# Kernel optimization log

Hardware: AMD Instinct MI355X
Metric: run time of the kernel (lower is better)

Reference implementation:

```python
import jax, jax.numpy as jnp
import numpy as np

B, TGT, SRC, H = 32, 512, 2048, 512


def setup_inputs() -> dict:
    key = jax.random.key(0)
    k1, k2, k3, k4, k5 = jax.random.split(key, 5)
    s = 1.0 / np.sqrt(H)
    return {
        "decoder_output": jax.random.normal(k1, (B, TGT, H), jnp.float32),
        "encoder_outputs": jax.random.normal(k2, (B, SRC, H), jnp.float32),
        # lengths in [SRC//2, SRC] so every row has at least one valid position
        "encoder_inputs_length": jax.random.randint(k3, (B,), SRC // 2, SRC + 1, jnp.int64),
        "W_in": jax.random.normal(k4, (H, H), jnp.float32) * s,   # linear_in weight (general)
        "W_out": jax.random.normal(k5, (H, 2 * H), jnp.float32) * s,  # linear_out weight, no bias
    }


def reference(decoder_output, encoder_outputs, encoder_inputs_length, W_in, W_out):
    # score (general): (q @ W_in^T) @ enc^T -> [B, tgt, src]
    q = jnp.einsum('bth,oh->bto', decoder_output, W_in)
    align = jnp.einsum('bth,bsh->bts', q, encoder_outputs)
    # mask positions j >= length with -inf, then softmax over src dim
    mask = jnp.arange(SRC)[None, None, :] < encoder_inputs_length[:, None, None]  # [B,1,src]
    align = jnp.where(mask, align, -jnp.inf)
    align_vectors = jax.nn.softmax(align, axis=2)  # [B, tgt, src]
    # context: [B, tgt, H]
    context = jnp.einsum('bts,bsh->bth', align_vectors, encoder_outputs)
    concat = jnp.concatenate([context, decoder_output], axis=2)  # [B, tgt, 2H]
    attn_h = jnp.tanh(jnp.einsum('btk,ok->bto', concat, W_out))  # [B, tgt, H]
    # transpose to [tgt, B, ...] as the torch module does
    return attn_h.transpose(1, 0, 2), align_vectors.transpose(1, 0, 2)
```

## Files before the change

kernel.cpp:

```cpp
#include <hip/hip_runtime.h>

#define Bc   32
#define TGTc 512
#define SRCc 2048
#define Hc   512

typedef unsigned short u16;
typedef unsigned int   u32;
typedef __attribute__((ext_vector_type(8))) short s16x8;
typedef __attribute__((ext_vector_type(4))) float f32x4;
typedef __attribute__((ext_vector_type(4))) unsigned short u16x4;

__device__ __forceinline__ u16 f2bf(float x) {
    u32 u = __float_as_uint(x);
    u32 r = (u + 0x7FFFu + ((u >> 16) & 1u)) >> 16;
    return (u16)r;
}
__device__ __forceinline__ float bf2f(u16 h) {
    return __uint_as_float(((u32)h) << 16);
}


__global__ void prep_len_k(const u32* __restrict__ raw, int* __restrict__ out) {
    int i = threadIdx.x;
    if (i >= Bc) return;
    bool is64 = (raw[1] == 0u);
    out[i] = (int)(is64 ? raw[2 * i] : raw[i]);
}

__global__ __launch_bounds__(256) void split_k(const float* __restrict__ in,
                                               u16* __restrict__ hi, u16* __restrict__ lo,
                                               int n4) {
    int stride = gridDim.x * 256;
    for (int i = blockIdx.x * 256 + threadIdx.x; i < n4; i += stride) {
        f32x4 x = ((const f32x4*)in)[i];
        u16x4 h, l;
#pragma unroll
        for (int j = 0; j < 4; j++) {
            u16 hb = f2bf(x[j]);
            h[j] = hb;
            l[j] = f2bf(x[j] - bf2f(hb));
        }
        ((u16x4*)hi)[i] = h;
        ((u16x4*)lo)[i] = l;
    }
}

__global__ __launch_bounds__(256) void split_wout_k(const float* __restrict__ in,
                                                    u16* __restrict__ ah, u16* __restrict__ al,
                                                    u16* __restrict__ bh, u16* __restrict__ bl) {
    int i = blockIdx.x * 256 + threadIdx.x;
    if (i >= 512 * 256) return;
    int o = i >> 8, kc = i & 255;
    f32x4 x = ((const f32x4*)in)[i];
    u16x4 h, l;
#pragma unroll
    for (int j = 0; j < 4; j++) {
        u16 hb = f2bf(x[j]);
        h[j] = hb;
        l[j] = f2bf(x[j] - bf2f(hb));
    }
    int half = kc >> 7;
    int idx = o * 128 + (kc & 127);
    ((u16x4*)(half ? bh : ah))[idx] = h;
    ((u16x4*)(half ? bl : al))[idx] = l;
}

__global__ __launch_bounds__(256) void prep_enc_k(const float* __restrict__ enc,
                                                  u16* __restrict__ ehi, u16* __restrict__ elo,
                                                  u16* __restrict__ ethi) {
    __shared__ float tile[32][33];
    const int b = blockIdx.z;
    const int s0 = blockIdx.x << 5, h0 = blockIdx.y << 5;
    const int x = threadIdx.x & 31, y = threadIdx.x >> 5;
    const long base = ((long)b * SRCc + s0) * Hc + h0;
#pragma unroll
    for (int j = 0; j < 4; j++) {
        int s = (y << 2) + j;
        float v = enc[base + (long)s * Hc + x];
        tile[s][x] = v;
        u16 h = f2bf(v);
        long o = base + (long)s * Hc + x;
        ehi[o] = h;
        elo[o] = f2bf(v - bf2f(h));
    }
    __syncthreads();
    const long tbase = ((long)b * Hc + h0) * SRCc + s0;
#pragma unroll
    for (int j = 0; j < 4; j++) {
        int hh = (y << 2) + j;
        float v = tile[x][hh];
        long o = tbase + (long)hh * SRCc + x;
        ethi[o] = f2bf(v);
    }
}


struct GArgs {
    const u16* A0; const u16* A1;
    const u16* B0; const u16* B1;
    void* out0; void* out1;
    const float* aux;
};

__device__ __forceinline__ void gload_lds16(const u16* g, u16* l) {
    __builtin_amdgcn_global_load_lds((const __attribute__((address_space(1))) void*)g,
                                     (__attribute__((address_space(3))) void*)l, 16, 0, 0);
}

template <int CFG>
__global__ __launch_bounds__(256, 2) void gemm_bt(GArgs g) {
    constexpr int NA = (CFG == 2) ? 1 : 2;
    constexpr int NB = (CFG == 2) ? 1 : 2;
    constexpr int NC = (CFG == 2) ? 1 : 3;
    constexpr int K  = (CFG == 2) ? 2048 : 512;
    constexpr int NT = NA + NB;

    __shared__ u16 lds[NT * 128 * 32];

    const int tid = threadIdx.x;
    const int lane = tid & 63;
    const int wave = tid >> 6;
    const int wm = wave >> 1;
    const int wn = wave & 1;

    int bz = 0, mt, nt;
    if constexpr (CFG == 1 || CFG == 2) { bz = blockIdx.x; mt = blockIdx.y; nt = blockIdx.z; }
    else { mt = blockIdx.x; nt = blockIdx.y; }

    const u16* ap[NA];
    const u16* bp[NB];
    if constexpr (CFG == 1) {
        const long ao = (long)bz * TGTc * Hc, bo = (long)bz * SRCc * Hc;
        ap[0] = g.A0 + ao; ap[1] = g.A1 + ao;
        bp[0] = g.B0 + bo; bp[1] = g.B1 + bo;
    } else if constexpr (CFG == 2) {
        ap[0] = g.A0 + (long)bz * TGTc * SRCc;
        bp[0] = g.B0 + (long)bz * Hc * SRCc;
    } else {
        ap[0] = g.A0; ap[1] = g.A1;
        bp[0] = g.B0; bp[1] = g.B1;
    }

    f32x4 acc[4][4];
#pragma unroll
    for (int mi = 0; mi < 4; mi++)
#pragma unroll
        for (int ni = 0; ni < 4; ni++)
            acc[mi][ni] = (f32x4){0.f, 0.f, 0.f, 0.f};

    const int arow0 = mt * 128;
    const int brow0 = nt * 128;

    constexpr int cAi[3] = {0, 0, 1};
    constexpr int cBi[3] = {0, 1, 0};

    for (int k0 = 0; k0 < K; k0 += 32) {
#pragma unroll
        for (int t = 0; t < NT; t++) {
            const u16* src = (t < NA) ? (ap[t] + (long)arow0 * K + k0)
                                      : (bp[t - NA] + (long)brow0 * K + k0);
            u16* dstbase = &lds[t * 4096];
#pragma unroll
            for (int it = 0; it < 2; ++it) {
                int l = it * 256 + tid;
                int row = l >> 2;
                int kel = (l & 3) << 3;
                gload_lds16(src + row * K + kel, dstbase + it * 2048 + wave * 512);
            }
        }
        __syncthreads();

        s16x8 af[NA][4];
        s16x8 bfr[NB][4];
#pragma unroll
        for (int i = 0; i < NA; i++)
#pragma unroll
            for (int f = 0; f < 4; f++) {
                int r = wm * 64 + f * 16 + (lane & 15);
                af[i][f] = *(const s16x8*)&lds[i * 4096 + r * 32 + ((lane >> 4) << 3)];
            }
#pragma unroll
        for (int i = 0; i < NB; i++)
#pragma unroll
            for (int f = 0; f < 4; f++) {
                int r = wn * 64 + f * 16 + (lane & 15);
                bfr[i][f] = *(const s16x8*)&lds[(NA + i) * 4096 + r * 32 + ((lane >> 4) << 3)];
            }

#pragma unroll
        for (int c = 0; c < NC; c++)
#pragma unroll
            for (int mi = 0; mi < 4; mi++)
#pragma unroll
                for (int ni = 0; ni < 4; ni++)
                    acc[mi][ni] = __builtin_amdgcn_mfma_f32_16x16x32_bf16(
                        af[cAi[c]][mi], bfr[cBi[c]][ni], acc[mi][ni], 0, 0, 0);
        __syncthreads();
    }

    const int m0 = mt * 128 + wm * 64;
    const int n0 = nt * 128 + wn * 64;
    const int ln15 = lane & 15;
    const int rg = (lane >> 4) << 2;

#pragma unroll
    for (int mi = 0; mi < 4; mi++) {
#pragma unroll
        for (int ni = 0; ni < 4; ni++) {
            f32x4 v = acc[mi][ni];
            int n = n0 + ni * 16 + ln15;
#pragma unroll
            for (int j = 0; j < 4; j++) {
                int m = m0 + mi * 16 + rg + j;
                float x = v[j];
                if constexpr (CFG == 0) {
                    long idx = (long)m * Hc + n;
                    u16 h = f2bf(x);
                    ((u16*)g.out0)[idx] = h;
                    ((u16*)g.out1)[idx] = f2bf(x - bf2f(h));
                } else if constexpr (CFG == 1) {
                    ((float*)g.out0)[((long)m * Bc + bz) * SRCc + n] = x;
                } else if constexpr (CFG == 2) {
                    long idx = ((long)bz * TGTc + m) * Hc + n;
                    u16 h = f2bf(x);
                    ((u16*)g.out0)[idx] = h;
                    ((u16*)g.out1)[idx] = f2bf(x - bf2f(h));
                } else if constexpr (CFG == 3) {
                    ((float*)g.out0)[(long)m * Hc + n] = x;
                } else {
                    float s = x + g.aux[(long)m * Hc + n];
                    float th = tanhf(s);
                    int t = m & (TGTc - 1), b = m >> 9;
                    ((float*)g.out0)[((long)t * Bc + b) * Hc + n] = th;
                }
            }
        }
    }
}

__global__ __launch_bounds__(256) void softmax_k(float* __restrict__ align, u16* __restrict__ Pb,
                                                 const int* __restrict__ lens) {
    const int row = blockIdx.x;
    const int b = row >> 9, t = row & (TGTc - 1);
    float* p = align + ((long)t * Bc + b) * SRCc;
    u16* pb = Pb + ((long)b * TGTc + t) * SRCc;
    const int len = lens[b];
    const int tid = threadIdx.x;

    f32x4 v[2];
    float mx = -3.4e38f;
#pragma unroll
    for (int i = 0; i < 2; i++) {
        int s0 = i * 1024 + tid * 4;
        v[i] = *(const f32x4*)&p[s0];
#pragma unroll
        for (int j = 0; j < 4; j++) {
            if (s0 + j >= len) v[i][j] = -3.4e38f;
            mx = fmaxf(mx, v[i][j]);
        }
    }
#pragma unroll
    for (int o = 32; o >= 1; o >>= 1) mx = fmaxf(mx, __shfl_xor(mx, o));
    __shared__ float red[8];
    if ((tid & 63) == 0) red[tid >> 6] = mx;
    __syncthreads();
    mx = fmaxf(fmaxf(red[0], red[1]), fmaxf(red[2], red[3]));

    float sum = 0.f;
    f32x4 e[2];
#pragma unroll
    for (int i = 0; i < 2; i++) {
        int s0 = i * 1024 + tid * 4;
#pragma unroll
        for (int j = 0; j < 4; j++) {
            float ev = (s0 + j >= len) ? 0.f : __expf(v[i][j] - mx);
            e[i][j] = ev;
            sum += ev;
        }
    }
#pragma unroll
    for (int o = 32; o >= 1; o >>= 1) sum += __shfl_xor(sum, o);
    if ((tid & 63) == 0) red[4 + (tid >> 6)] = sum;
    __syncthreads();
    sum = (red[4] + red[5]) + (red[6] + red[7]);
    float inv = 1.f / sum;

#pragma unroll
    for (int i = 0; i < 2; i++) {
        int s0 = i * 1024 + tid * 4;
        f32x4 o4;
        u16x4 h4;
#pragma unroll
        for (int j = 0; j < 4; j++) {
            float pv = e[i][j] * inv;
            o4[j] = pv;
            h4[j] = f2bf(pv);
        }
        *(f32x4*)&p[s0] = o4;
        *(u16x4*)&pb[s0] = h4;
    }
}


extern "C" void kernel_launch(void* const* d_in, const int* in_sizes, int n_in,
                              void* d_out, int out_size, void* d_ws, size_t ws_size,
                              hipStream_t stream) {
    const float* dec  = (const float*)d_in[0];
    const float* enc  = (const float*)d_in[1];
    const u32*   lenp = (const u32*)d_in[2];
    const float* win  = (const float*)d_in[3];
    const float* wout = (const float*)d_in[4];

    float* out_attn  = (float*)d_out;
    float* out_align = out_attn + (size_t)TGTc * Bc * Hc;

    char* w = (char*)d_ws;
    auto take = [&](size_t n) { char* p = w; w += (n + 255) & ~(size_t)255; return p; };
    int* lens      = (int*)take(256);
    u16* dec_hi    = (u16*)take((size_t)8388608 * 2);
    u16* dec_lo    = (u16*)take((size_t)8388608 * 2);
    u16* win_hi    = (u16*)take((size_t)262144 * 2);
    u16* win_lo    = (u16*)take((size_t)262144 * 2);
    u16* wA_hi     = (u16*)take((size_t)262144 * 2);
    u16* wA_lo     = (u16*)take((size_t)262144 * 2);
    u16* wB_hi     = (u16*)take((size_t)262144 * 2);
    u16* wB_lo     = (u16*)take((size_t)262144 * 2);
    float* partial = (float*)take((size_t)8388608 * 4);
    u16* enc_hi    = (u16*)take((size_t)33554432 * 2);
    u16* enc_lo    = (u16*)take((size_t)33554432 * 2);
    u16* encT_hi   = (u16*)take((size_t)33554432 * 2);
    u16* q_hi   = (u16*)out_attn;
    u16* q_lo   = q_hi + 8388608;
    u16* Pb     = enc_hi;
    u16* ctx_hi = enc_lo;
    u16* ctx_lo = enc_lo + 8388608;
    (void)in_sizes; (void)n_in; (void)out_size; (void)ws_size;

    prep_len_k<<<1, 64, 0, stream>>>(lenp, lens);
    split_k<<<2048, 256, 0, stream>>>(dec, dec_hi, dec_lo, 8388608 / 4);
    split_k<<<256, 256, 0, stream>>>(win, win_hi, win_lo, 262144 / 4);
    split_wout_k<<<512, 256, 0, stream>>>(wout, wA_hi, wA_lo, wB_hi, wB_lo);
    prep_enc_k<<<dim3(64, 16, 32), 256, 0, stream>>>(enc, enc_hi, enc_lo, encT_hi);

    GArgs a1 = {};
    a1.A0 = dec_hi; a1.A1 = dec_lo; a1.B0 = win_hi; a1.B1 = win_lo;
    a1.out0 = q_hi; a1.out1 = q_lo;
    gemm_bt<0><<<dim3(128, 4, 1), 256, 0, stream>>>(a1);

    GArgs a2 = {};
    a2.A0 = q_hi; a2.A1 = q_lo; a2.B0 = enc_hi; a2.B1 = enc_lo;
    a2.out0 = out_align;
    gemm_bt<1><<<dim3(32, 4, 16), 256, 0, stream>>>(a2);

    softmax_k<<<16384, 256, 0, stream>>>(out_align, Pb, lens);

    GArgs a4 = {};
    a4.A0 = Pb; a4.B0 = encT_hi;
    a4.out0 = ctx_hi; a4.out1 = ctx_lo;
    gemm_bt<2><<<dim3(32, 4, 4), 256, 0, stream>>>(a4);

    GArgs a5 = {};
    a5.A0 = ctx_hi; a5.A1 = ctx_lo; a5.B0 = wA_hi; a5.B1 = wA_lo;
    a5.out0 = partial;
    gemm_bt<3><<<dim3(128, 4, 1), 256, 0, stream>>>(a5);

    GArgs a6 = {};
    a6.A0 = dec_hi; a6.A1 = dec_lo; a6.B0 = wB_hi; a6.B1 = wB_lo;
    a6.out0 = out_attn; a6.aux = partial;
    gemm_bt<4><<<dim3(128, 4, 1), 256, 0, stream>>>(a6);
}
```

Baseline: 684.8 us.

## Fuse output projection GEMMs, swizzle LDS, reorder grid, raise occupancy

```diff
diff --git a/kernel.cpp b/kernel.cpp
--- a/kernel.cpp
+++ b/kernel.cpp
@@ -99,8 +99,9 @@
 struct GArgs {
     const u16* A0; const u16* A1;
     const u16* B0; const u16* B1;
+    const u16* A2; const u16* A3;
+    const u16* B2; const u16* B3;
     void* out0; void* out1;
-    const float* aux;
 };
 
 __device__ __forceinline__ void gload_lds16(const u16* g, u16* l) {
@@ -109,11 +110,12 @@
 }
 
 template <int CFG>
-__global__ __launch_bounds__(256, 2) void gemm_bt(GArgs g) {
+__global__ __launch_bounds__(256, 3) void gemm_bt(GArgs g) {
     constexpr int NA = (CFG == 2) ? 1 : 2;
     constexpr int NB = (CFG == 2) ? 1 : 2;
     constexpr int NC = (CFG == 2) ? 1 : 3;
-    constexpr int K  = (CFG == 2) ? 2048 : 512;
+    constexpr int K  = (CFG == 2) ? 2048 : (CFG == 3 ? 1024 : 512);
+    constexpr int KST = (CFG == 3) ? 512 : K;
     constexpr int NT = NA + NB;
 
     __shared__ u16 lds[NT * 128 * 32];
@@ -125,21 +127,24 @@
     const int wn = wave & 1;
 
     int bz = 0, mt, nt;
-    if constexpr (CFG == 1 || CFG == 2) { bz = blockIdx.x; mt = blockIdx.y; nt = blockIdx.z; }
+    if constexpr (CFG == 1 || CFG == 2) { bz = blockIdx.z; mt = blockIdx.y; nt = blockIdx.x; }
     else { mt = blockIdx.x; nt = blockIdx.y; }
 
-    const u16* ap[NA];
-    const u16* bp[NB];
+    const u16* apt[2][2];
+    const u16* bpt[2][2];
     if constexpr (CFG == 1) {
         const long ao = (long)bz * TGTc * Hc, bo = (long)bz * SRCc * Hc;
-        ap[0] = g.A0 + ao; ap[1] = g.A1 + ao;
-        bp[0] = g.B0 + bo; bp[1] = g.B1 + bo;
+        apt[0][0] = g.A0 + ao; apt[0][1] = g.A1 + ao;
+        bpt[0][0] = g.B0 + bo; bpt[0][1] = g.B1 + bo;
     } else if constexpr (CFG == 2) {
-        ap[0] = g.A0 + (long)bz * TGTc * SRCc;
-        bp[0] = g.B0 + (long)bz * Hc * SRCc;
+        apt[0][0] = g.A0 + (long)bz * TGTc * SRCc;
+        bpt[0][0] = g.B0 + (long)bz * Hc * SRCc;
+    } else if constexpr (CFG == 3) {
+        apt[0][0] = g.A0; apt[0][1] = g.A1; apt[1][0] = g.A2; apt[1][1] = g.A3;
+        bpt[0][0] = g.B0; bpt[0][1] = g.B1; bpt[1][0] = g.B2; bpt[1][1] = g.B3;
     } else {
-        ap[0] = g.A0; ap[1] = g.A1;
-        bp[0] = g.B0; bp[1] = g.B1;
+        apt[0][0] = g.A0; apt[0][1] = g.A1;
+        bpt[0][0] = g.B0; bpt[0][1] = g.B1;
     }
 
     f32x4 acc[4][4];
@@ -155,18 +160,22 @@
     constexpr int cAi[3] = {0, 0, 1};
     constexpr int cBi[3] = {0, 1, 0};
 
+    const int csw = (((lane >> 4) ^ (lane & 3)) << 3);
+
     for (int k0 = 0; k0 < K; k0 += 32) {
+        int sel = 0, kk = k0;
+        if constexpr (CFG == 3) { sel = k0 >> 9; kk = k0 & 511; }
 #pragma unroll
         for (int t = 0; t < NT; t++) {
-            const u16* src = (t < NA) ? (ap[t] + (long)arow0 * K + k0)
-                                      : (bp[t - NA] + (long)brow0 * K + k0);
+            const u16* base = (t < NA) ? (apt[sel][t] + (long)arow0 * KST + kk)
+                                       : (bpt[sel][t - NA] + (long)brow0 * KST + kk);
             u16* dstbase = &lds[t * 4096];
 #pragma unroll
             for (int it = 0; it < 2; ++it) {
                 int l = it * 256 + tid;
                 int row = l >> 2;
-                int kel = (l & 3) << 3;
-                gload_lds16(src + row * K + kel, dstbase + it * 2048 + wave * 512);
+                int kel = ((l & 3) ^ (row & 3)) << 3;
+                gload_lds16(base + (long)row * KST + kel, dstbase + it * 2048 + wave * 512);
             }
         }
         __syncthreads();
@@ -178,14 +187,14 @@
 #pragma unroll
             for (int f = 0; f < 4; f++) {
                 int r = wm * 64 + f * 16 + (lane & 15);
-                af[i][f] = *(const s16x8*)&lds[i * 4096 + r * 32 + ((lane >> 4) << 3)];
+                af[i][f] = *(const s16x8*)&lds[i * 4096 + r * 32 + csw];
             }
 #pragma unroll
         for (int i = 0; i < NB; i++)
 #pragma unroll
             for (int f = 0; f < 4; f++) {
                 int r = wn * 64 + f * 16 + (lane & 15);
-                bfr[i][f] = *(const s16x8*)&lds[(NA + i) * 4096 + r * 32 + ((lane >> 4) << 3)];
+                bfr[i][f] = *(const s16x8*)&lds[(NA + i) * 4096 + r * 32 + csw];
             }
 
 #pragma unroll
@@ -226,11 +235,8 @@
                     u16 h = f2bf(x);
                     ((u16*)g.out0)[idx] = h;
                     ((u16*)g.out1)[idx] = f2bf(x - bf2f(h));
-                } else if constexpr (CFG == 3) {
-                    ((float*)g.out0)[(long)m * Hc + n] = x;
                 } else {
-                    float s = x + g.aux[(long)m * Hc + n];
-                    float th = tanhf(s);
+                    float th = tanhf(x);
                     int t = m & (TGTc - 1), b = m >> 9;
                     ((float*)g.out0)[((long)t * Bc + b) * Hc + n] = th;
                 }
@@ -326,7 +332,6 @@
     u16* wA_lo     = (u16*)take((size_t)262144 * 2);
     u16* wB_hi     = (u16*)take((size_t)262144 * 2);
     u16* wB_lo     = (u16*)take((size_t)262144 * 2);
-    float* partial = (float*)take((size_t)8388608 * 4);
     u16* enc_hi    = (u16*)take((size_t)33554432 * 2);
     u16* enc_lo    = (u16*)take((size_t)33554432 * 2);
     u16* encT_hi   = (u16*)take((size_t)33554432 * 2);
@@ -351,22 +356,18 @@
     GArgs a2 = {};
     a2.A0 = q_hi; a2.A1 = q_lo; a2.B0 = enc_hi; a2.B1 = enc_lo;
     a2.out0 = out_align;
-    gemm_bt<1><<<dim3(32, 4, 16), 256, 0, stream>>>(a2);
+    gemm_bt<1><<<dim3(16, 4, 32), 256, 0, stream>>>(a2);
 
     softmax_k<<<16384, 256, 0, stream>>>(out_align, Pb, lens);
 
     GArgs a4 = {};
     a4.A0 = Pb; a4.B0 = encT_hi;
     a4.out0 = ctx_hi; a4.out1 = ctx_lo;
-    gemm_bt<2><<<dim3(32, 4, 4), 256, 0, stream>>>(a4);
+    gemm_bt<2><<<dim3(4, 4, 32), 256, 0, stream>>>(a4);
 
     GArgs a5 = {};
     a5.A0 = ctx_hi; a5.A1 = ctx_lo; a5.B0 = wA_hi; a5.B1 = wA_lo;
-    a5.out0 = partial;
+    a5.A2 = dec_hi; a5.A3 = dec_lo; a5.B2 = wB_hi; a5.B3 = wB_lo;
+    a5.out0 = out_attn;
     gemm_bt<3><<<dim3(128, 4, 1), 256, 0, stream>>>(a5);
-
-    GArgs a6 = {};
-    a6.A0 = dec_hi; a6.A1 = dec_lo; a6.B0 = wB_hi; a6.B1 = wB_lo;
-    a6.out0 = out_attn; a6.aux = partial;
-    gemm_bt<4><<<dim3(128, 4, 1), 256, 0, stream>>>(a6);
-}
+}
```

Result: no change. 671.8 us (-1.9%).
